# Kernel optimization log

Hardware: AMD Instinct MI355X
Metric: run time of the kernel (lower is better)

The kernel has to match this reference:

```python
import jax, jax.numpy as jnp
import numpy as np

N_NODES = 16384
N_EDGES = 262144
D_IN = 256
D = 256          # out_feats == d_model
H = 512          # d_inner = 2*d_model
E = 64           # moe_num_expert
TOP_K = 2
CAP = 1024       # expert capacity = 2 * N*K / E (generous, no drops in practice)
BN_EPS = 1e-5


def setup_inputs() -> dict:
    key = jax.random.key(0)
    ks = jax.random.split(key, 16)
    s = lambda d: 1.0 / np.sqrt(d)
    inp = {
        "feats": jax.random.normal(ks[0], (N_NODES, D_IN), jnp.float32),
        "W_gc": jax.random.normal(ks[1], (D_IN, D), jnp.float32) * s(D_IN),
        "b_gc": jnp.zeros((D,), jnp.float32),
        "W_res": jax.random.normal(ks[2], (D_IN, D), jnp.float32) * s(D_IN),
        "b_res": jnp.zeros((D,), jnp.float32),
        "Wg": jax.random.normal(ks[3], (D, E), jnp.float32) * s(D),
        "bg": jnp.zeros((E,), jnp.float32),
        "w1": jax.random.normal(ks[4], (E, D, H), jnp.float32) * s(D),
        "b1": jnp.zeros((E, H), jnp.float32),
        "w2": jax.random.normal(ks[5], (E, H, D), jnp.float32) * s(H),
        "b2": jnp.zeros((E, D), jnp.float32),
        "gamma": jnp.ones((D,), jnp.float32),
        "beta": jnp.zeros((D,), jnp.float32),
        "src": jax.random.randint(ks[6], (N_EDGES,), 0, N_NODES),
        "dst": jax.random.randint(ks[7], (N_EDGES,), 0, N_NODES),
    }
    return inp


def _moe_ff(x, Wg, bg, w1, b1, w2, b2):
    """Top-2 MoE FFN (FMoE NaiveGate semantics): softmax over selected top-k logits."""
    N = x.shape[0]
    logits = x @ Wg + bg                                   # [N, E]
    vals, idx = jax.lax.top_k(logits, TOP_K)               # [N, K]
    gates = jax.nn.softmax(vals, axis=-1)                  # [N, K]

    e_flat = idx.reshape(-1)                               # [N*K]
    g_flat = gates.reshape(-1)
    tok = jnp.arange(N * TOP_K) // TOP_K                   # token id per pair

    order = jnp.argsort(e_flat)                            # stable sort by expert
    e_s, tok_s, g_s = e_flat[order], tok[order], g_flat[order]
    counts = jnp.bincount(e_flat, length=E)
    offs = jnp.concatenate([jnp.zeros((1,), counts.dtype), jnp.cumsum(counts)[:-1]])
    rank = jnp.arange(N * TOP_K) - offs[e_s]               # position within expert
    valid = rank < CAP
    slot = jnp.where(valid, e_s * CAP + rank, E * CAP)     # overflow -> dummy row

    buf = jnp.zeros((E * CAP + 1, D), x.dtype).at[slot].set(x[tok_s])
    h = buf[: E * CAP].reshape(E, CAP, D)
    h1 = jax.nn.gelu(jnp.einsum("ecd,edh->ech", h, w1) + b1[:, None, :], approximate=False)
    h2 = jnp.einsum("ech,ehd->ecd", h1, w2) + b2[:, None, :]
    out_buf = h2.reshape(E * CAP, D)

    y_s = jnp.where(valid[:, None], out_buf[jnp.minimum(slot, E * CAP - 1)], 0.0)
    return jnp.zeros((N, D), x.dtype).at[tok_s].add(g_s[:, None] * y_s)


def _forward(feats, W_gc, b_gc, W_res, b_res, Wg, bg, w1, b1, w2, b2, gamma, beta, src, dst):
    n = feats.shape[0]
    ones = jnp.ones((src.shape[0],), feats.dtype)
    deg_out = jnp.clip(jax.ops.segment_sum(ones, src, num_segments=n), 1.0)
    deg_in = jnp.clip(jax.ops.segment_sum(ones, dst, num_segments=n), 1.0)
    # symmetric-normalized GCN aggregation over edge list
    h = feats * jax.lax.rsqrt(deg_out)[:, None]
    m = jax.ops.segment_sum(h[src], dst, num_segments=n) * jax.lax.rsqrt(deg_in)[:, None]
    gc = m @ W_gc + b_gc
    x = gc + (feats @ W_res + b_res)                       # residual branch (dropout p=0)

    core = _moe_ff(x, Wg, bg, w1, b1, w2, b2)
    y = x + core                                           # pre-BN residual
    mean = jnp.mean(y, axis=0)
    var = jnp.mean((y - mean) ** 2, axis=0)                # biased var (torch BN train)
    return (y - mean) * jax.lax.rsqrt(var + BN_EPS) * gamma + beta


def reference(feats, W_gc, b_gc, W_res, b_res, Wg, bg, w1, b1, w2, b2, gamma, beta, src, dst):
    return _forward(feats, W_gc, b_gc, W_res, b_res, Wg, bg, w1, b1, w2, b2, gamma, beta, src, dst)
```

## Files before the change

### kernel.cpp

```cpp
#include <hip/hip_runtime.h>
#include <math.h>

static const int kN     = 16384;
static const int kEdges = 262144;
static const int kD     = 256;
static const int kH     = 512;
static const int kE     = 64;
static const int kCap   = 1024;
static const int kPairs = kN * 2;

static const size_t OFF_DEGO    = 0;
static const size_t OFF_DEGI    = OFF_DEGO + 65536;
static const size_t OFF_CURSOR  = OFF_DEGI + 65536;
static const size_t OFF_ECOUNT  = OFF_CURSOR + 65536;
static const size_t OFF_ECUR    = OFF_ECOUNT + 256;
static const size_t OFF_COLSUM  = OFF_ECUR + 256;
static const size_t OFF_COLSUM2 = OFF_COLSUM + 1024;
static const size_t ZERO_BYTES  = OFF_COLSUM2 + 1024;
static const size_t OFF_EOFFS   = ZERO_BYTES;
static const size_t OFF_CSROFF  = OFF_EOFFS + 512;
static const size_t OFF_CSRSRC  = OFF_CSROFF + 65792;
static const size_t OFF_PLIST   = OFF_CSRSRC + 1048576;
static const size_t OFF_EIDX    = OFF_PLIST + 131072;
static const size_t OFF_EGATE   = OFF_EIDX + 131072;
static const size_t OFF_SCALE   = OFF_EGATE + 131072;
static const size_t OFF_SHIFT   = OFF_SCALE + 1024;
static const size_t OFF_OSC     = OFF_SHIFT + 1024;
static const size_t OFF_ISC     = OFF_OSC + 65536;
static const size_t OFF_WQ1     = OFF_ISC + 65536;
static const size_t OFF_WQ2     = OFF_WQ1 + 65536;
static const size_t OFF_BGE     = OFF_WQ2 + 65536;
static const size_t OFF_WCAT    = OFF_BGE + 256;
static const size_t OFF_M       = OFF_WCAT + 262144;
static const size_t OFF_X       = OFF_M + 16777216;
static const size_t OFF_XB      = OFF_X + 16777216;
static const size_t OFF_LOGITS  = OFF_XB + 8388608;
static const size_t OFF_POUT    = OFF_LOGITS + 4194304;
static const size_t OFF_W1T     = OFF_POUT + 16777216;
static const size_t OFF_W2T     = OFF_W1T + 16777216;
static const size_t OFF_H1B     = OFF_W2T + 16777216;
static const size_t OFF_PART1   = OFF_H1B + 33554432;
static const size_t OFF_PART2   = OFF_PART1 + 262144;

typedef __bf16 bfrag __attribute__((ext_vector_type(8)));
typedef float f32x4 __attribute__((ext_vector_type(4)));

__device__ __forceinline__ float gelu_f(float v) {
    float u = v * (0.7978845608f + 0.0356774081f * v * v);
    float t = __expf(-2.0f * fabsf(u));
    float th = (1.0f - t) * __builtin_amdgcn_rcpf(1.0f + t);
    th = copysignf(th, u);
    return 0.5f * v * (1.0f + th);
}
__device__ __forceinline__ unsigned short f2bf(float f) {
    union { float f; unsigned int u; } v; v.f = f;
    unsigned int u = v.u;
    unsigned int r = (u + 0x7FFFu + ((u >> 16) & 1u)) >> 16;
    return (unsigned short)r;
}
__device__ __forceinline__ float bf2f(unsigned short s) {
    union { unsigned int u; float f; } v; v.u = ((unsigned int)s) << 16;
    return v.f;
}

__global__ __launch_bounds__(256) void k_count_deg(const int* __restrict__ src,
                                                   const int* __restrict__ dst,
                                                   int* __restrict__ dego,
                                                   int* __restrict__ degi) {
    int i = blockIdx.x * 256 + threadIdx.x;
    if (i < kEdges) {
        atomicAdd(&dego[src[i]], 1);
        atomicAdd(&degi[dst[i]], 1);
    }
}

__global__ __launch_bounds__(256) void k_scales(const int* __restrict__ dego,
                                                const int* __restrict__ degi,
                                                float* __restrict__ osc,
                                                float* __restrict__ isc) {
    int i = blockIdx.x * 256 + threadIdx.x;
    int a = dego[i]; if (a < 1) a = 1;
    int b = degi[i]; if (b < 1) b = 1;
    osc[i] = rsqrtf((float)a);
    isc[i] = rsqrtf((float)b);
}

__global__ __launch_bounds__(1024) void k_scan_nodes(const int* __restrict__ degi,
                                                     int* __restrict__ offs) {
    __shared__ int sums[1024];
    int t = threadIdx.x;
    int base = t * 16;
    int loc[16];
    int s = 0;
#pragma unroll
    for (int i = 0; i < 16; ++i) { loc[i] = degi[base + i]; s += loc[i]; }
    sums[t] = s;
    __syncthreads();
    for (int off = 1; off < 1024; off <<= 1) {
        int v = (t >= off) ? sums[t - off] : 0;
        __syncthreads();
        sums[t] += v;
        __syncthreads();
    }
    int run = sums[t] - s;
#pragma unroll
    for (int i = 0; i < 16; ++i) { offs[base + i] = run; run += loc[i]; }
    if (t == 1023) offs[kN] = run;
}

__global__ __launch_bounds__(256) void k_build_csr(const int* __restrict__ src,
                                                   const int* __restrict__ dst,
                                                   const int* __restrict__ offs,
                                                   int* __restrict__ cursor,
                                                   int* __restrict__ csr_src) {
    int i = blockIdx.x * 256 + threadIdx.x;
    if (i < kEdges) {
        int d = dst[i];
        int pos = atomicAdd(&cursor[d], 1);
        csr_src[offs[d] + pos] = src[i];
    }
}

__global__ __launch_bounds__(256) void k_aggregate(const float* __restrict__ feats,
                                                   const float* __restrict__ osc,
                                                   const float* __restrict__ isc,
                                                   const int* __restrict__ offs,
                                                   const int* __restrict__ csr_src,
                                                   float* __restrict__ m) {
    __shared__ f32x4 red[256];
    int n = blockIdx.x;
    int t = threadIdx.x;
    int c4 = (t & 63) * 4;
    int es = t >> 6;
    int beg = offs[n], end = offs[n + 1];
    f32x4 acc = {0.f, 0.f, 0.f, 0.f};
    for (int i = beg + es; i < end; i += 4) {
        int s = csr_src[i];
        float sc = osc[s];
        const float4 v = *(const float4*)(feats + (size_t)s * kD + c4);
        acc[0] += v.x * sc; acc[1] += v.y * sc;
        acc[2] += v.z * sc; acc[3] += v.w * sc;
    }
    red[t] = acc;
    __syncthreads();
    if (t < 64) {
        f32x4 a = red[t], b = red[t + 64], c = red[t + 128], d = red[t + 192];
        float si = isc[n];
        float4 o;
        o.x = (a[0] + b[0] + c[0] + d[0]) * si;
        o.y = (a[1] + b[1] + c[1] + d[1]) * si;
        o.z = (a[2] + b[2] + c[2] + d[2]) * si;
        o.w = (a[3] + b[3] + c[3] + d[3]) * si;
        *(float4*)(m + (size_t)n * kD + c4) = o;
    }
}

__global__ __launch_bounds__(256) void k_compose(const float* __restrict__ Wgc,
                                                 const float* __restrict__ Wres,
                                                 const float* __restrict__ Wg,
                                                 const float* __restrict__ bgc,
                                                 const float* __restrict__ bres,
                                                 const float* __restrict__ bg,
                                                 float* __restrict__ Wq1,
                                                 float* __restrict__ Wq2,
                                                 float* __restrict__ bge) {
    int tid = blockIdx.x * 256 + threadIdx.x;
    if (tid < 2 * kD * kE) {
        int mat = tid >> 14;
        int rem = tid & 16383;
        int d = rem >> 6, e = rem & 63;
        const float* A = mat ? Wres : Wgc;
        float acc = 0.f;
        for (int c = 0; c < kD; ++c)
            acc = fmaf(A[d * kD + c], Wg[c * kE + e], acc);
        (mat ? Wq2 : Wq1)[d * kE + e] = acc;
    } else if (tid < 2 * kD * kE + kE) {
        int e = tid - 2 * kD * kE;
        float acc = bg[e];
        for (int d = 0; d < kD; ++d)
            acc = fmaf(bgc[d] + bres[d], Wg[d * kE + e], acc);
        bge[e] = acc;
    }
}

#define FMA16()                                                                         \
    acc[0][0]=fmaf(a.x,b.x,acc[0][0]); acc[0][1]=fmaf(a.x,b.y,acc[0][1]);               \
    acc[0][2]=fmaf(a.x,b.z,acc[0][2]); acc[0][3]=fmaf(a.x,b.w,acc[0][3]);               \
    acc[1][0]=fmaf(a.y,b.x,acc[1][0]); acc[1][1]=fmaf(a.y,b.y,acc[1][1]);               \
    acc[1][2]=fmaf(a.y,b.z,acc[1][2]); acc[1][3]=fmaf(a.y,b.w,acc[1][3]);               \
    acc[2][0]=fmaf(a.z,b.x,acc[2][0]); acc[2][1]=fmaf(a.z,b.y,acc[2][1]);               \
    acc[2][2]=fmaf(a.z,b.z,acc[2][2]); acc[2][3]=fmaf(a.z,b.w,acc[2][3]);               \
    acc[3][0]=fmaf(a.w,b.x,acc[3][0]); acc[3][1]=fmaf(a.w,b.y,acc[3][1]);               \
    acc[3][2]=fmaf(a.w,b.z,acc[3][2]); acc[3][3]=fmaf(a.w,b.w,acc[3][3]);

__global__ __launch_bounds__(256) void k_gate_comp(const float* __restrict__ m,
                                                   const float* __restrict__ feats,
                                                   const float* __restrict__ Wq1,
                                                   const float* __restrict__ Wq2,
                                                   const float* __restrict__ bge,
                                                   float* __restrict__ logits) {
    __shared__ float As[32][68];
    __shared__ float Bs[32][68];
    const int t = threadIdx.x;
    const int tx = t & 15, ty = t >> 4;
    const int m0 = blockIdx.y * 64;
    float acc[4][4] = {};
    for (int pass = 0; pass < 2; ++pass) {
        const float* A = pass ? feats : m;
        const float* B = pass ? Wq2 : Wq1;
        for (int kb = 0; kb < kD; kb += 32) {
            __syncthreads();
#pragma unroll
            for (int i = 0; i < 2; ++i) {
                int fidx = i * 256 + t;
                int r = fidx >> 3, k4 = fidx & 7;
                float4 v = *(const float4*)(A + (size_t)(m0 + r) * kD + kb + k4 * 4);
                As[k4 * 4 + 0][r] = v.x; As[k4 * 4 + 1][r] = v.y;
                As[k4 * 4 + 2][r] = v.z; As[k4 * 4 + 3][r] = v.w;
            }
#pragma unroll
            for (int i = 0; i < 2; ++i) {
                int fidx = i * 256 + t;
                int kk = fidx >> 4, c4 = fidx & 15;
                float4 v = *(const float4*)(B + (size_t)(kb + kk) * kE + c4 * 4);
                *(float4*)&Bs[kk][c4 * 4] = v;
            }
            __syncthreads();
#pragma unroll
            for (int kk = 0; kk < 32; ++kk) {
                float4 a = *(const float4*)&As[kk][ty * 4];
                float4 b = *(const float4*)&Bs[kk][tx * 4];
                FMA16();
            }
        }
    }
    int col0 = tx * 4;
    float4 bb = *(const float4*)(bge + col0);
#pragma unroll
    for (int i = 0; i < 4; ++i) {
        int row = m0 + ty * 4 + i;
        float4 o;
        o.x = acc[i][0] + bb.x; o.y = acc[i][1] + bb.y;
        o.z = acc[i][2] + bb.z; o.w = acc[i][3] + bb.w;
        *(float4*)(logits + (size_t)row * kE + col0) = o;
    }
}

__global__ __launch_bounds__(256) void k_cast_cat(const float* __restrict__ m,
                                                  const float* __restrict__ feats,
                                                  unsigned short* __restrict__ acat) {
    int i = blockIdx.x * 256 + threadIdx.x;
    const float* srcp = blockIdx.y ? feats : m;
    int doff = blockIdx.y ? 256 : 0;
    size_t g = (size_t)i * 8;
    int tok = (int)(g >> 8), d = (int)(g & 255);
    float4 a = *(const float4*)(srcp + g);
    float4 b = *(const float4*)(srcp + g + 4);
    ushort4 o0, o1;
    o0.x = f2bf(a.x); o0.y = f2bf(a.y); o0.z = f2bf(a.z); o0.w = f2bf(a.w);
    o1.x = f2bf(b.x); o1.y = f2bf(b.y); o1.z = f2bf(b.z); o1.w = f2bf(b.w);
    unsigned short* dstp = acat + (size_t)tok * 512 + doff + d;
    *(ushort4*)dstp = o0;
    *(ushort4*)(dstp + 4) = o1;
}

__global__ __launch_bounds__(256) void k_transpose_cast(const float* __restrict__ w,
                                                        unsigned short* __restrict__ wt,
                                                        int R, int C, int dstride, int doff) {
    __shared__ unsigned short tile[64][65];
    int e = blockIdx.z;
    const float* W = w + (size_t)e * R * C;
    unsigned short* WT = wt + (size_t)e * R * C;
    int r0 = blockIdx.y * 64, c0 = blockIdx.x * 64;
    int t = threadIdx.x;
#pragma unroll
    for (int i = 0; i < 4; ++i) {
        int idx = i * 256 + t;
        int r = idx >> 4, c4 = idx & 15;
        float4 v = *(const float4*)(W + (size_t)(r0 + r) * C + c0 + c4 * 4);
        tile[r][c4 * 4 + 0] = f2bf(v.x); tile[r][c4 * 4 + 1] = f2bf(v.y);
        tile[r][c4 * 4 + 2] = f2bf(v.z); tile[r][c4 * 4 + 3] = f2bf(v.w);
    }
    __syncthreads();
#pragma unroll
    for (int i = 0; i < 4; ++i) {
        int idx = i * 256 + t;
        int c = idx >> 4, r4 = idx & 15;
        ushort4 o;
        o.x = tile[r4 * 4 + 0][c]; o.y = tile[r4 * 4 + 1][c];
        o.z = tile[r4 * 4 + 2][c]; o.w = tile[r4 * 4 + 3][c];
        *(ushort4*)(WT + (size_t)(c0 + c) * dstride + doff + r0 + r4 * 4) = o;
    }
}

__global__ __launch_bounds__(256) void k_xgemm_mfma(const unsigned short* __restrict__ acat,
                                                    const unsigned short* __restrict__ wcat,
                                                    const float* __restrict__ bgc,
                                                    const float* __restrict__ bres,
                                                    float* __restrict__ x,
                                                    unsigned short* __restrict__ xb) {
    __shared__ unsigned short As[128 * 32];
    __shared__ unsigned short Bs[128 * 32];
    const int t = threadIdx.x;
    const int m0 = blockIdx.y * 128;
    const int n0 = blockIdx.x * 128;
    const int lane = t & 63, w = t >> 6;
    const int m_off = (w & 1) * 64, n_off = (w >> 1) * 64;
    const int quad = lane >> 4, lr = lane & 15;
    float breg[4];
#pragma unroll
    for (int ni = 0; ni < 4; ++ni) {
        int col = n0 + n_off + ni * 16 + lr;
        breg[ni] = bgc[col] + bres[col];
    }
    const int arow0 = t >> 2, arow1 = 64 + (t >> 2);
    const int kseg = (t & 3) * 8;
    const unsigned short* pA0 = acat + (size_t)(m0 + arow0) * 512 + kseg;
    const unsigned short* pA1 = acat + (size_t)(m0 + arow1) * 512 + kseg;
    const unsigned short* pB0 = wcat + (size_t)(n0 + arow0) * 512 + kseg;
    const unsigned short* pB1 = wcat + (size_t)(n0 + arow1) * 512 + kseg;
    unsigned short* sA0 = &As[arow0 * 32 + kseg];
    unsigned short* sA1 = &As[arow1 * 32 + kseg];
    unsigned short* sB0 = &Bs[arow0 * 32 + kseg];
    unsigned short* sB1 = &Bs[arow1 * 32 + kseg];
    f32x4 acc[4][4] = {};
    for (int kb = 0; kb < 512; kb += 32) {
        uint4 a0 = *(const uint4*)(pA0 + kb);
        uint4 a1 = *(const uint4*)(pA1 + kb);
        uint4 bv0 = *(const uint4*)(pB0 + kb);
        uint4 bv1 = *(const uint4*)(pB1 + kb);
        __syncthreads();
        *(uint4*)sA0 = a0; *(uint4*)sA1 = a1;
        *(uint4*)sB0 = bv0; *(uint4*)sB1 = bv1;
        __syncthreads();
        bfrag af[4], bf[4];
#pragma unroll
        for (int mi = 0; mi < 4; ++mi)
            af[mi] = *(const bfrag*)&As[(m_off + mi * 16 + lr) * 32 + quad * 8];
#pragma unroll
        for (int ni = 0; ni < 4; ++ni)
            bf[ni] = *(const bfrag*)&Bs[(n_off + ni * 16 + lr) * 32 + quad * 8];
#pragma unroll
        for (int mi = 0; mi < 4; ++mi)
#pragma unroll
            for (int ni = 0; ni < 4; ++ni)
                acc[mi][ni] = __builtin_amdgcn_mfma_f32_16x16x32_bf16(af[mi], bf[ni], acc[mi][ni], 0, 0, 0);
    }
#pragma unroll
    for (int mi = 0; mi < 4; ++mi) {
#pragma unroll
        for (int r = 0; r < 4; ++r) {
            int row = m0 + m_off + mi * 16 + quad * 4 + r;
            float* xrow = x + (size_t)row * kD + n0 + n_off + lr;
            unsigned short* xbrow = xb + (size_t)row * kD + n0 + n_off + lr;
#pragma unroll
            for (int ni = 0; ni < 4; ++ni) {
                float v = acc[mi][ni][r] + breg[ni];
                xrow[ni * 16] = v;
                xbrow[ni * 16] = f2bf(v);
            }
        }
    }
}

__global__ __launch_bounds__(256) void k_topk(const float* __restrict__ logits,
                                              int* __restrict__ eidx,
                                              float* __restrict__ egate,
                                              int* __restrict__ ecount) {
    __shared__ int hist[kE];
    int t = threadIdx.x;
    int n = blockIdx.x * 256 + t;
    if (t < kE) hist[t] = 0;
    __syncthreads();
    const float* row = logits + (size_t)n * kE;
    float v0 = -3.4e38f, v1 = -3.4e38f;
    int i0 = 0, i1 = 0;
    for (int e4 = 0; e4 < kE; e4 += 4) {
        float4 vv = *(const float4*)(row + e4);
        float vs[4] = {vv.x, vv.y, vv.z, vv.w};
#pragma unroll
        for (int j = 0; j < 4; ++j) {
            float v = vs[j];
            int e = e4 + j;
            if (v > v0) { v1 = v0; i1 = i0; v0 = v; i0 = e; }
            else if (v > v1) { v1 = v; i1 = e; }
        }
    }
    float ex = expf(v1 - v0);
    float g0 = 1.0f / (1.0f + ex);
    float g1 = ex * g0;
    eidx[2 * n] = i0; eidx[2 * n + 1] = i1;
    egate[2 * n] = g0; egate[2 * n + 1] = g1;
    atomicAdd(&hist[i0], 1);
    atomicAdd(&hist[i1], 1);
    __syncthreads();
    if (t < kE) {
        int c = hist[t];
        if (c > 0) atomicAdd(&ecount[t], c);
    }
}

__global__ void k_scan_experts(const int* __restrict__ ecount, int* __restrict__ eoffs) {
    if (threadIdx.x == 0) {
        int s = 0;
        for (int e = 0; e < kE; ++e) { eoffs[e] = s; s += ecount[e]; }
        eoffs[kE] = s;
    }
}

__global__ __launch_bounds__(256) void k_scatter(const int* __restrict__ eidx,
                                                 const int* __restrict__ eoffs,
                                                 int* __restrict__ ecur,
                                                 int* __restrict__ plist) {
    __shared__ int lh[kE];
    __shared__ int gbase[kE];
    int t = threadIdx.x;
    int p0 = blockIdx.x * 512 + t;
    if (t < kE) lh[t] = 0;
    __syncthreads();
    int e0 = eidx[p0], e1 = eidx[p0 + 256];
    atomicAdd(&lh[e0], 1);
    atomicAdd(&lh[e1], 1);
    __syncthreads();
    if (t < kE) {
        int c = lh[t];
        int b = (c > 0) ? atomicAdd(&ecur[t], c) : 0;
        gbase[t] = eoffs[t] + b;
        lh[t] = 0;
    }
    __syncthreads();
    int r0 = atomicAdd(&lh[e0], 1);
    int r1 = atomicAdd(&lh[e1], 1);
    plist[gbase[e0] + r0] = p0;
    plist[gbase[e1] + r1] = p0 + 256;
}

__global__ __launch_bounds__(256) void k_moe1_mfma(const unsigned short* __restrict__ xb,
                                                   const unsigned short* __restrict__ w1t,
                                                   const float* __restrict__ b1,
                                                   const int* __restrict__ plist,
                                                   const int* __restrict__ eoffs,
                                                   const int* __restrict__ ecount,
                                                   unsigned short* __restrict__ h1b) {
    __shared__ unsigned short As[128 * 32];
    __shared__ unsigned short Bs[128 * 32];
    __shared__ int rowtok[128];
    const int e = blockIdx.z;
    int cnt = ecount[e]; if (cnt > kCap) cnt = kCap;
    const int m0 = blockIdx.y * 128;
    if (m0 >= cnt) return;
    const int n0 = blockIdx.x * 128;
    const int base = eoffs[e];
    const int t = threadIdx.x;
    if (t < 128) {
        int slot = m0 + t;
        rowtok[t] = (slot < cnt) ? (plist[base + slot] >> 1) : -1;
    }
    const int lane = t & 63, w = t >> 6;
    const int m_off = (w & 1) * 64, n_off = (w >> 1) * 64;
    const int quad = lane >> 4, lr = lane & 15;
    const unsigned short* Bbase = w1t + (size_t)e * kH * kD;
    float breg[4];
#pragma unroll
    for (int ni = 0; ni < 4; ++ni) breg[ni] = b1[e * kH + n0 + n_off + ni * 16 + lr];
    const int arow0 = t >> 2, arow1 = 64 + (t >> 2);
    const int kseg = (t & 3) * 8;
    __syncthreads();
    const int tok0 = rowtok[arow0], tok1 = rowtok[arow1];
    const unsigned short* pA0 = (tok0 >= 0) ? xb + (size_t)tok0 * kD + kseg : nullptr;
    const unsigned short* pA1 = (tok1 >= 0) ? xb + (size_t)tok1 * kD + kseg : nullptr;
    const unsigned short* pB0 = Bbase + (size_t)(n0 + arow0) * kD + kseg;
    const unsigned short* pB1 = Bbase + (size_t)(n0 + arow1) * kD + kseg;
    unsigned short* sA0 = &As[arow0 * 32 + kseg];
    unsigned short* sA1 = &As[arow1 * 32 + kseg];
    unsigned short* sB0 = &Bs[arow0 * 32 + kseg];
    unsigned short* sB1 = &Bs[arow1 * 32 + kseg];
    f32x4 acc[4][4] = {};
    for (int kb = 0; kb < kD; kb += 32) {
        uint4 a0 = pA0 ? *(const uint4*)(pA0 + kb) : make_uint4(0, 0, 0, 0);
        uint4 a1 = pA1 ? *(const uint4*)(pA1 + kb) : make_uint4(0, 0, 0, 0);
        uint4 bv0 = *(const uint4*)(pB0 + kb);
        uint4 bv1 = *(const uint4*)(pB1 + kb);
        __syncthreads();
        *(uint4*)sA0 = a0; *(uint4*)sA1 = a1;
        *(uint4*)sB0 = bv0; *(uint4*)sB1 = bv1;
        __syncthreads();
        bfrag af[4], bf[4];
#pragma unroll
        for (int mi = 0; mi < 4; ++mi)
            af[mi] = *(const bfrag*)&As[(m_off + mi * 16 + lr) * 32 + quad * 8];
#pragma unroll
        for (int ni = 0; ni < 4; ++ni)
            bf[ni] = *(const bfrag*)&Bs[(n_off + ni * 16 + lr) * 32 + quad * 8];
#pragma unroll
        for (int mi = 0; mi < 4; ++mi)
#pragma unroll
            for (int ni = 0; ni < 4; ++ni)
                acc[mi][ni] = __builtin_amdgcn_mfma_f32_16x16x32_bf16(af[mi], bf[ni], acc[mi][ni], 0, 0, 0);
    }
#pragma unroll
    for (int mi = 0; mi < 4; ++mi) {
#pragma unroll
        for (int r = 0; r < 4; ++r) {
            int slot = m0 + m_off + mi * 16 + quad * 4 + r;
            if (slot < cnt) {
                unsigned short* orow = h1b + (size_t)(base + slot) * kH + n0 + n_off + lr;
#pragma unroll
                for (int ni = 0; ni < 4; ++ni)
                    orow[ni * 16] = f2bf(gelu_f(acc[mi][ni][r] + breg[ni]));
            }
        }
    }
}

__global__ __launch_bounds__(256) void k_moe2_mfma(const unsigned short* __restrict__ h1b,
                                                   const unsigned short* __restrict__ w2t,
                                                   const float* __restrict__ b2,
                                                   const int* __restrict__ plist,
                                                   const int* __restrict__ eoffs,
                                                   const int* __restrict__ ecount,
                                                   const float* __restrict__ egate,
                                                   unsigned short* __restrict__ pout) {
    __shared__ unsigned short As[128 * 32];
    __shared__ unsigned short Bs[128 * 32];
    __shared__ int prow[128];
    __shared__ float sgate[128];
    const int e = blockIdx.z;
    int cnt = ecount[e]; if (cnt > kCap) cnt = kCap;
    const int m0 = blockIdx.y * 128;
    if (m0 >= cnt) return;
    const int n0 = blockIdx.x * 128;
    const int base = eoffs[e];
    const int t = threadIdx.x;
    if (t < 128) {
        int slot = m0 + t;
        int p = (slot < cnt) ? plist[base + slot] : -1;
        prow[t] = p;
        sgate[t] = (p >= 0) ? egate[p] : 0.f;
    }
    const int lane = t & 63, w = t >> 6;
    const int m_off = (w & 1) * 64, n_off = (w >> 1) * 64;
    const int quad = lane >> 4, lr = lane & 15;
    const unsigned short* Bbase = w2t + (size_t)e * kD * kH;
    float breg[4];
#pragma unroll
    for (int ni = 0; ni < 4; ++ni) breg[ni] = b2[e * kD + n0 + n_off + ni * 16 + lr];
    const int arow0 = t >> 2, arow1 = 64 + (t >> 2);
    const int kseg = (t & 3) * 8;
    int aslot0 = m0 + arow0, aslot1 = m0 + arow1;
    const unsigned short* pA0 = (aslot0 < cnt) ? h1b + (size_t)(base + aslot0) * kH + kseg : nullptr;
    const unsigned short* pA1 = (aslot1 < cnt) ? h1b + (size_t)(base + aslot1) * kH + kseg : nullptr;
    const unsigned short* pB0 = Bbase + (size_t)(n0 + arow0) * kH + kseg;
    const unsigned short* pB1 = Bbase + (size_t)(n0 + arow1) * kH + kseg;
    unsigned short* sA0 = &As[arow0 * 32 + kseg];
    unsigned short* sA1 = &As[arow1 * 32 + kseg];
    unsigned short* sB0 = &Bs[arow0 * 32 + kseg];
    unsigned short* sB1 = &Bs[arow1 * 32 + kseg];
    f32x4 acc[4][4] = {};
    for (int kb = 0; kb < kH; kb += 32) {
        uint4 a0 = pA0 ? *(const uint4*)(pA0 + kb) : make_uint4(0, 0, 0, 0);
        uint4 a1 = pA1 ? *(const uint4*)(pA1 + kb) : make_uint4(0, 0, 0, 0);
        uint4 bv0 = *(const uint4*)(pB0 + kb);
        uint4 bv1 = *(const uint4*)(pB1 + kb);
        __syncthreads();
        *(uint4*)sA0 = a0; *(uint4*)sA1 = a1;
        *(uint4*)sB0 = bv0; *(uint4*)sB1 = bv1;
        __syncthreads();
        bfrag af[4], bf[4];
#pragma unroll
        for (int mi = 0; mi < 4; ++mi)
            af[mi] = *(const bfrag*)&As[(m_off + mi * 16 + lr) * 32 + quad * 8];
#pragma unroll
        for (int ni = 0; ni < 4; ++ni)
            bf[ni] = *(const bfrag*)&Bs[(n_off + ni * 16 + lr) * 32 + quad * 8];
#pragma unroll
        for (int mi = 0; mi < 4; ++mi)
#pragma unroll
            for (int ni = 0; ni < 4; ++ni)
                acc[mi][ni] = __builtin_amdgcn_mfma_f32_16x16x32_bf16(af[mi], bf[ni], acc[mi][ni], 0, 0, 0);
    }
#pragma unroll
    for (int mi = 0; mi < 4; ++mi) {
#pragma unroll
        for (int r = 0; r < 4; ++r) {
            int lslot = m_off + mi * 16 + quad * 4 + r;
            int p = prow[lslot];
            if (p >= 0) {
                float g = sgate[lslot];
                unsigned short* orow = pout + (size_t)p * kD + n0 + n_off + lr;
#pragma unroll
                for (int ni = 0; ni < 4; ++ni)
                    orow[ni * 16] = f2bf(g * (acc[mi][ni][r] + breg[ni]));
            }
        }
    }
}

__global__ __launch_bounds__(256) void k_colsum(const float* __restrict__ x,
                                                const unsigned short* __restrict__ pout,
                                                float* __restrict__ part1,
                                                float* __restrict__ part2) {
    int d = threadIdx.x;
    int r0 = blockIdx.x * 64;
    float s = 0.f, s2 = 0.f;
    for (int i = 0; i < 64; ++i) {
        int row = r0 + i;
        float v = x[(size_t)row * kD + d]
                + bf2f(pout[(size_t)(2 * row) * kD + d])
                + bf2f(pout[(size_t)(2 * row + 1) * kD + d]);
        s += v; s2 += v * v;
    }
    part1[blockIdx.x * kD + d] = s;
    part2[blockIdx.x * kD + d] = s2;
}

__global__ void k_bnparams(const float* __restrict__ part1,
                           const float* __restrict__ part2,
                           const float* __restrict__ gamma,
                           const float* __restrict__ beta,
                           float* __restrict__ scale,
                           float* __restrict__ shift) {
    int d = threadIdx.x;
    float s = 0.f, s2 = 0.f;
    for (int b = 0; b < 256; ++b) {
        s += part1[b * kD + d];
        s2 += part2[b * kD + d];
    }
    float mean = s * (1.0f / kN);
    float var = s2 * (1.0f / kN) - mean * mean;
    float inv = rsqrtf(var + 1e-5f);
    float sc = inv * gamma[d];
    scale[d] = sc;
    shift[d] = beta[d] - mean * sc;
}

__global__ __launch_bounds__(256) void k_apply2(const float* __restrict__ x,
                                                const unsigned short* __restrict__ pout,
                                                const float* __restrict__ scale,
                                                const float* __restrict__ shift,
                                                float* __restrict__ out) {
    int i = blockIdx.x * 256 + threadIdx.x;
    size_t g = (size_t)i * 4;
    int row = (int)(g >> 8);
    int d = (int)(g & 255);
    float4 v = *(const float4*)(x + g);
    ushort4 p0 = *(const ushort4*)(pout + (size_t)(2 * row) * kD + d);
    ushort4 p1 = *(const ushort4*)(pout + (size_t)(2 * row + 1) * kD + d);
    v.x += bf2f(p0.x) + bf2f(p1.x);
    v.y += bf2f(p0.y) + bf2f(p1.y);
    v.z += bf2f(p0.z) + bf2f(p1.z);
    v.w += bf2f(p0.w) + bf2f(p1.w);
    float4 sc = *(const float4*)(scale + d);
    float4 sh = *(const float4*)(shift + d);
    v.x = v.x * sc.x + sh.x;
    v.y = v.y * sc.y + sh.y;
    v.z = v.z * sc.z + sh.z;
    v.w = v.w * sc.w + sh.w;
    *(float4*)(out + g) = v;
}

extern "C" void kernel_launch(void* const* d_in, const int* in_sizes, int n_in,
                              void* d_out, int out_size, void* d_ws, size_t ws_size,
                              hipStream_t stream) {
    const float* feats = (const float*)d_in[0];
    const float* Wgc   = (const float*)d_in[1];
    const float* bgc   = (const float*)d_in[2];
    const float* Wres  = (const float*)d_in[3];
    const float* bres  = (const float*)d_in[4];
    const float* Wg    = (const float*)d_in[5];
    const float* bg    = (const float*)d_in[6];
    const float* w1    = (const float*)d_in[7];
    const float* b1    = (const float*)d_in[8];
    const float* w2    = (const float*)d_in[9];
    const float* b2    = (const float*)d_in[10];
    const float* gamma = (const float*)d_in[11];
    const float* beta  = (const float*)d_in[12];
    const int*   src   = (const int*)d_in[13];
    const int*   dst   = (const int*)d_in[14];

    char* ws = (char*)d_ws;
    int*   dego    = (int*)(ws + OFF_DEGO);
    int*   degi    = (int*)(ws + OFF_DEGI);
    int*   cursor  = (int*)(ws + OFF_CURSOR);
    int*   ecount  = (int*)(ws + OFF_ECOUNT);
    int*   ecur    = (int*)(ws + OFF_ECUR);
    int*   eoffs   = (int*)(ws + OFF_EOFFS);
    int*   csroff  = (int*)(ws + OFF_CSROFF);
    int*   csrsrc  = (int*)(ws + OFF_CSRSRC);
    int*   plist   = (int*)(ws + OFF_PLIST);
    int*   eidx    = (int*)(ws + OFF_EIDX);
    float* egate   = (float*)(ws + OFF_EGATE);
    float* scale   = (float*)(ws + OFF_SCALE);
    float* shift   = (float*)(ws + OFF_SHIFT);
    float* osc     = (float*)(ws + OFF_OSC);
    float* iscv    = (float*)(ws + OFF_ISC);
    float* Wq1     = (float*)(ws + OFF_WQ1);
    float* Wq2     = (float*)(ws + OFF_WQ2);
    float* bge     = (float*)(ws + OFF_BGE);
    unsigned short* wcat = (unsigned short*)(ws + OFF_WCAT);
    float* mbuf    = (float*)(ws + OFF_M);
    float* xbuf    = (float*)(ws + OFF_X);
    unsigned short* xb   = (unsigned short*)(ws + OFF_XB);
    float* logits  = (float*)(ws + OFF_LOGITS);
    unsigned short* pout = (unsigned short*)(ws + OFF_POUT);
    unsigned short* acat = (unsigned short*)(ws + OFF_POUT);
    unsigned short* w1t  = (unsigned short*)(ws + OFF_W1T);
    unsigned short* w2t  = (unsigned short*)(ws + OFF_W2T);
    unsigned short* h1b  = (unsigned short*)(ws + OFF_H1B);
    float* part1   = (float*)(ws + OFF_PART1);
    float* part2   = (float*)(ws + OFF_PART2);

    hipMemsetAsync(ws, 0, ZERO_BYTES, stream);

    k_transpose_cast<<<dim3(kH / 64, kD / 64, kE), 256, 0, stream>>>(w1, w1t, kD, kH, kD, 0);
    k_transpose_cast<<<dim3(kD / 64, kH / 64, kE), 256, 0, stream>>>(w2, w2t, kH, kD, kH, 0);
    k_transpose_cast<<<dim3(kD / 64, kD / 64, 1), 256, 0, stream>>>(Wgc, wcat, kD, kD, 512, 0);
    k_transpose_cast<<<dim3(kD / 64, kD / 64, 1), 256, 0, stream>>>(Wres, wcat, kD, kD, 512, 256);
    k_compose<<<129, 256, 0, stream>>>(Wgc, Wres, Wg, bgc, bres, bg, Wq1, Wq2, bge);
    k_count_deg<<<kEdges / 256, 256, 0, stream>>>(src, dst, dego, degi);
    k_scales<<<kN / 256, 256, 0, stream>>>(dego, degi, osc, iscv);
    k_scan_nodes<<<1, 1024, 0, stream>>>(degi, csroff);
    k_build_csr<<<kEdges / 256, 256, 0, stream>>>(src, dst, csroff, cursor, csrsrc);
    k_aggregate<<<kN, 256, 0, stream>>>(feats, osc, iscv, csroff, csrsrc, mbuf);
    k_gate_comp<<<dim3(1, kN / 64), 256, 0, stream>>>(mbuf, feats, Wq1, Wq2, bge, logits);
    k_cast_cat<<<dim3(kN * kD / 8 / 256, 2), 256, 0, stream>>>(mbuf, feats, acat);
    k_xgemm_mfma<<<dim3(kD / 128, kN / 128), 256, 0, stream>>>(acat, wcat, bgc, bres, xbuf, xb);
    k_topk<<<kN / 256, 256, 0, stream>>>(logits, eidx, egate, ecount);
    k_scan_experts<<<1, 64, 0, stream>>>(ecount, eoffs);
    k_scatter<<<kPairs / 512, 256, 0, stream>>>(eidx, eoffs, ecur, plist);
    k_moe1_mfma<<<dim3(kH / 128, kCap / 128, kE), 256, 0, stream>>>(xb, w1t, b1, plist, eoffs, ecount, h1b);
    k_moe2_mfma<<<dim3(kD / 128, kCap / 128, kE), 256, 0, stream>>>(h1b, w2t, b2, plist, eoffs, ecount, egate, pout);
    k_colsum<<<kN / 64, 256, 0, stream>>>(xbuf, pout, part1, part2);
    k_bnparams<<<1, 256, 0, stream>>>(part1, part2, gamma, beta, scale, shift);
    k_apply2<<<(kN * kD / 4) / 256, 256, 0, stream>>>(xbuf, pout, scale, shift, (float*)d_out);
}
```

Baseline: 414.2 us.

## Use direct global-to-LDS loads with swizzled 64-wide K tiles in GEMMs, fuse cast into aggregate

The three MFMA GEMMs now stage A and B tiles with global_load_lds straight into LDS, using a K tile of 64 and an XOR swizzle to avoid bank conflicts. Padding rows read from a zeroed workspace row, so the null-pointer branches are gone. The aggregation kernel now uses 512 threads and writes the bf16 copy of m directly, with a separate small kernel casting feats, which removes the combined cast pass over m. The trade-offs are twice the LDS per block, which may lower occupancy, and a loop that is still not double-buffered.

```diff
diff --git a/kernel.cpp b/kernel.cpp
--- a/kernel.cpp
+++ b/kernel.cpp
@@ -14,9 +14,8 @@
 static const size_t OFF_CURSOR  = OFF_DEGI + 65536;
 static const size_t OFF_ECOUNT  = OFF_CURSOR + 65536;
 static const size_t OFF_ECUR    = OFF_ECOUNT + 256;
-static const size_t OFF_COLSUM  = OFF_ECUR + 256;
-static const size_t OFF_COLSUM2 = OFF_COLSUM + 1024;
-static const size_t ZERO_BYTES  = OFF_COLSUM2 + 1024;
+static const size_t OFF_ZROW    = OFF_ECUR + 256;
+static const size_t ZERO_BYTES  = OFF_ZROW + 2048;
 static const size_t OFF_EOFFS   = ZERO_BYTES;
 static const size_t OFF_CSROFF  = OFF_EOFFS + 512;
 static const size_t OFF_CSRSRC  = OFF_CSROFF + 65792;
@@ -45,6 +44,12 @@
 typedef __bf16 bfrag __attribute__((ext_vector_type(8)));
 typedef float f32x4 __attribute__((ext_vector_type(4)));
 
+__device__ __forceinline__ void gll16(const void* g, void* l) {
+    __builtin_amdgcn_global_load_lds(
+        (const __attribute__((address_space(1))) unsigned int*)g,
+        (__attribute__((address_space(3))) unsigned int*)l, 16, 0, 0);
+}
+
 __device__ __forceinline__ float gelu_f(float v) {
     float u = v * (0.7978845608f + 0.0356774081f * v * v);
     float t = __expf(-2.0f * fabsf(u));
@@ -121,20 +126,21 @@
     }
 }
 
-__global__ __launch_bounds__(256) void k_aggregate(const float* __restrict__ feats,
+__global__ __launch_bounds__(512) void k_aggregate(const float* __restrict__ feats,
                                                    const float* __restrict__ osc,
                                                    const float* __restrict__ isc,
                                                    const int* __restrict__ offs,
                                                    const int* __restrict__ csr_src,
-                                                   float* __restrict__ m) {
-    __shared__ f32x4 red[256];
+                                                   float* __restrict__ m,
+                                                   unsigned short* __restrict__ acat) {
+    __shared__ f32x4 red[512];
     int n = blockIdx.x;
     int t = threadIdx.x;
     int c4 = (t & 63) * 4;
     int es = t >> 6;
     int beg = offs[n], end = offs[n + 1];
     f32x4 acc = {0.f, 0.f, 0.f, 0.f};
-    for (int i = beg + es; i < end; i += 4) {
+    for (int i = beg + es; i < end; i += 8) {
         int s = csr_src[i];
         float sc = osc[s];
         const float4 v = *(const float4*)(feats + (size_t)s * kD + c4);
@@ -144,15 +150,35 @@
     red[t] = acc;
     __syncthreads();
     if (t < 64) {
-        f32x4 a = red[t], b = red[t + 64], c = red[t + 128], d = red[t + 192];
+        f32x4 a = red[t];
+#pragma unroll
+        for (int j = 1; j < 8; ++j) {
+            f32x4 b = red[t + 64 * j];
+            a[0] += b[0]; a[1] += b[1]; a[2] += b[2]; a[3] += b[3];
+        }
         float si = isc[n];
         float4 o;
-        o.x = (a[0] + b[0] + c[0] + d[0]) * si;
-        o.y = (a[1] + b[1] + c[1] + d[1]) * si;
-        o.z = (a[2] + b[2] + c[2] + d[2]) * si;
-        o.w = (a[3] + b[3] + c[3] + d[3]) * si;
+        o.x = a[0] * si; o.y = a[1] * si; o.z = a[2] * si; o.w = a[3] * si;
         *(float4*)(m + (size_t)n * kD + c4) = o;
-    }
+        ushort4 ob;
+        ob.x = f2bf(o.x); ob.y = f2bf(o.y); ob.z = f2bf(o.z); ob.w = f2bf(o.w);
+        *(ushort4*)(acat + (size_t)n * 512 + c4) = ob;
+    }
+}
+
+__global__ __launch_bounds__(256) void k_cast_feats(const float* __restrict__ feats,
+                                                    unsigned short* __restrict__ acat) {
+    int i = blockIdx.x * 256 + threadIdx.x;
+    size_t g = (size_t)i * 8;
+    int tok = (int)(g >> 8), d = (int)(g & 255);
+    float4 a = *(const float4*)(feats + g);
+    float4 b = *(const float4*)(feats + g + 4);
+    ushort4 o0, o1;
+    o0.x = f2bf(a.x); o0.y = f2bf(a.y); o0.z = f2bf(a.z); o0.w = f2bf(a.w);
+    o1.x = f2bf(b.x); o1.y = f2bf(b.y); o1.z = f2bf(b.z); o1.w = f2bf(b.w);
+    unsigned short* dstp = acat + (size_t)tok * 512 + 256 + d;
+    *(ushort4*)dstp = o0;
+    *(ushort4*)(dstp + 4) = o1;
 }
 
 __global__ __launch_bounds__(256) void k_compose(const float* __restrict__ Wgc,
@@ -246,24 +272,6 @@
     }
 }
 
-__global__ __launch_bounds__(256) void k_cast_cat(const float* __restrict__ m,
-                                                  const float* __restrict__ feats,
-                                                  unsigned short* __restrict__ acat) {
-    int i = blockIdx.x * 256 + threadIdx.x;
-    const float* srcp = blockIdx.y ? feats : m;
-    int doff = blockIdx.y ? 256 : 0;
-    size_t g = (size_t)i * 8;
-    int tok = (int)(g >> 8), d = (int)(g & 255);
-    float4 a = *(const float4*)(srcp + g);
-    float4 b = *(const float4*)(srcp + g + 4);
-    ushort4 o0, o1;
-    o0.x = f2bf(a.x); o0.y = f2bf(a.y); o0.z = f2bf(a.z); o0.w = f2bf(a.w);
-    o1.x = f2bf(b.x); o1.y = f2bf(b.y); o1.z = f2bf(b.z); o1.w = f2bf(b.w);
-    unsigned short* dstp = acat + (size_t)tok * 512 + doff + d;
-    *(ushort4*)dstp = o0;
-    *(ushort4*)(dstp + 4) = o1;
-}
-
 __global__ __launch_bounds__(256) void k_transpose_cast(const float* __restrict__ w,
                                                         unsigned short* __restrict__ wt,
                                                         int R, int C, int dstride, int doff) {
@@ -299,11 +307,10 @@
                                                     const float* __restrict__ bres,
                                                     float* __restrict__ x,
                                                     unsigned short* __restrict__ xb) {
-    __shared__ unsigned short As[128 * 32];
-    __shared__ unsigned short Bs[128 * 32];
+    __shared__ unsigned short As[128 * 64];
+    __shared__ unsigned short Bs[128 * 64];
     const int t = threadIdx.x;
-    const int m0 = blockIdx.y * 128;
-    const int n0 = blockIdx.x * 128;
+    const int m0 = blockIdx.y * 128, n0 = blockIdx.x * 128;
     const int lane = t & 63, w = t >> 6;
     const int m_off = (w & 1) * 64, n_off = (w >> 1) * 64;
     const int quad = lane >> 4, lr = lane & 15;
@@ -313,38 +320,37 @@
         int col = n0 + n_off + ni * 16 + lr;
         breg[ni] = bgc[col] + bres[col];
     }
-    const int arow0 = t >> 2, arow1 = 64 + (t >> 2);
-    const int kseg = (t & 3) * 8;
-    const unsigned short* pA0 = acat + (size_t)(m0 + arow0) * 512 + kseg;
-    const unsigned short* pA1 = acat + (size_t)(m0 + arow1) * 512 + kseg;
-    const unsigned short* pB0 = wcat + (size_t)(n0 + arow0) * 512 + kseg;
-    const unsigned short* pB1 = wcat + (size_t)(n0 + arow1) * 512 + kseg;
-    unsigned short* sA0 = &As[arow0 * 32 + kseg];
-    unsigned short* sA1 = &As[arow1 * 32 + kseg];
-    unsigned short* sB0 = &Bs[arow0 * 32 + kseg];
-    unsigned short* sB1 = &Bs[arow1 * 32 + kseg];
+    const int lsub = lane >> 3, lslot = lane & 7;
+    const int swz8 = (lslot ^ lsub) * 8;
+    const unsigned short* pAb = acat + (size_t)(m0 + w * 8 + lsub) * 512 + swz8;
+    const unsigned short* pBb = wcat + (size_t)(n0 + w * 8 + lsub) * 512 + swz8;
+    unsigned short* sA = As + w * 8 * 64;
+    unsigned short* sB = Bs + w * 8 * 64;
     f32x4 acc[4][4] = {};
-    for (int kb = 0; kb < 512; kb += 32) {
-        uint4 a0 = *(const uint4*)(pA0 + kb);
-        uint4 a1 = *(const uint4*)(pA1 + kb);
-        uint4 bv0 = *(const uint4*)(pB0 + kb);
-        uint4 bv1 = *(const uint4*)(pB1 + kb);
+    for (int kb = 0; kb < 512; kb += 64) {
         __syncthreads();
-        *(uint4*)sA0 = a0; *(uint4*)sA1 = a1;
-        *(uint4*)sB0 = bv0; *(uint4*)sB1 = bv1;
+#pragma unroll
+        for (int j = 0; j < 4; ++j) {
+            gll16(pAb + (size_t)j * 32 * 512 + kb, sA + j * 2048);
+            gll16(pBb + (size_t)j * 32 * 512 + kb, sB + j * 2048);
+        }
         __syncthreads();
-        bfrag af[4], bf[4];
-#pragma unroll
-        for (int mi = 0; mi < 4; ++mi)
-            af[mi] = *(const bfrag*)&As[(m_off + mi * 16 + lr) * 32 + quad * 8];
-#pragma unroll
-        for (int ni = 0; ni < 4; ++ni)
-            bf[ni] = *(const bfrag*)&Bs[(n_off + ni * 16 + lr) * 32 + quad * 8];
-#pragma unroll
-        for (int mi = 0; mi < 4; ++mi)
+#pragma unroll
+        for (int h = 0; h < 2; ++h) {
+            const int soff = ((h * 4 + quad) ^ (lr & 7)) * 8;
+            bfrag af[4], bf[4];
+#pragma unroll
+            for (int mi = 0; mi < 4; ++mi)
+                af[mi] = *(const bfrag*)&As[(m_off + mi * 16 + lr) * 64 + soff];
 #pragma unroll
             for (int ni = 0; ni < 4; ++ni)
-                acc[mi][ni] = __builtin_amdgcn_mfma_f32_16x16x32_bf16(af[mi], bf[ni], acc[mi][ni], 0, 0, 0);
+                bf[ni] = *(const bfrag*)&Bs[(n_off + ni * 16 + lr) * 64 + soff];
+#pragma unroll
+            for (int mi = 0; mi < 4; ++mi)
+#pragma unroll
+                for (int ni = 0; ni < 4; ++ni)
+                    acc[mi][ni] = __builtin_amdgcn_mfma_f32_16x16x32_bf16(af[mi], bf[ni], acc[mi][ni], 0, 0, 0);
+        }
     }
 #pragma unroll
     for (int mi = 0; mi < 4; ++mi) {
@@ -441,9 +447,10 @@
                                                    const int* __restrict__ plist,
                                                    const int* __restrict__ eoffs,
                                                    const int* __restrict__ ecount,
+                                                   const unsigned short* __restrict__ zrow,
                                                    unsigned short* __restrict__ h1b) {
-    __shared__ unsigned short As[128 * 32];
-    __shared__ unsigned short Bs[128 * 32];
+    __shared__ unsigned short As[128 * 64];
+    __shared__ unsigned short Bs[128 * 64];
     __shared__ int rowtok[128];
     const int e = blockIdx.z;
     int cnt = ecount[e]; if (cnt > kCap) cnt = kCap;
@@ -463,40 +470,44 @@
     float breg[4];
 #pragma unroll
     for (int ni = 0; ni < 4; ++ni) breg[ni] = b1[e * kH + n0 + n_off + ni * 16 + lr];
-    const int arow0 = t >> 2, arow1 = 64 + (t >> 2);
-    const int kseg = (t & 3) * 8;
-    __syncthreads();
-    const int tok0 = rowtok[arow0], tok1 = rowtok[arow1];
-    const unsigned short* pA0 = (tok0 >= 0) ? xb + (size_t)tok0 * kD + kseg : nullptr;
-    const unsigned short* pA1 = (tok1 >= 0) ? xb + (size_t)tok1 * kD + kseg : nullptr;
-    const unsigned short* pB0 = Bbase + (size_t)(n0 + arow0) * kD + kseg;
-    const unsigned short* pB1 = Bbase + (size_t)(n0 + arow1) * kD + kseg;
-    unsigned short* sA0 = &As[arow0 * 32 + kseg];
-    unsigned short* sA1 = &As[arow1 * 32 + kseg];
-    unsigned short* sB0 = &Bs[arow0 * 32 + kseg];
-    unsigned short* sB1 = &Bs[arow1 * 32 + kseg];
+    const int lsub = lane >> 3, lslot = lane & 7;
+    const int swz8 = (lslot ^ lsub) * 8;
+    __syncthreads();
+    const unsigned short* pA[4];
+#pragma unroll
+    for (int j = 0; j < 4; ++j) {
+        int r = w * 8 + j * 32 + lsub;
+        int tok = rowtok[r];
+        pA[j] = (tok >= 0) ? (xb + (size_t)tok * kD + swz8) : (zrow + swz8);
+    }
+    const unsigned short* pBb = Bbase + (size_t)(n0 + w * 8 + lsub) * kD + swz8;
+    unsigned short* sA = As + w * 8 * 64;
+    unsigned short* sB = Bs + w * 8 * 64;
     f32x4 acc[4][4] = {};
-    for (int kb = 0; kb < kD; kb += 32) {
-        uint4 a0 = pA0 ? *(const uint4*)(pA0 + kb) : make_uint4(0, 0, 0, 0);
-        uint4 a1 = pA1 ? *(const uint4*)(pA1 + kb) : make_uint4(0, 0, 0, 0);
-        uint4 bv0 = *(const uint4*)(pB0 + kb);
-        uint4 bv1 = *(const uint4*)(pB1 + kb);
+    for (int kb = 0; kb < kD; kb += 64) {
         __syncthreads();
-        *(uint4*)sA0 = a0; *(uint4*)sA1 = a1;
-        *(uint4*)sB0 = bv0; *(uint4*)sB1 = bv1;
+#pragma unroll
+        for (int j = 0; j < 4; ++j) {
+            gll16(pA[j] + kb, sA + j * 2048);
+            gll16(pBb + (size_t)j * 32 * kD + kb, sB + j * 2048);
+        }
         __syncthreads();
-        bfrag af[4], bf[4];
-#pragma unroll
-        for (int mi = 0; mi < 4; ++mi)
-            af[mi] = *(const bfrag*)&As[(m_off + mi * 16 + lr) * 32 + quad * 8];
-#pragma unroll
-        for (int ni = 0; ni < 4; ++ni)
-            bf[ni] = *(const bfrag*)&Bs[(n_off + ni * 16 + lr) * 32 + quad * 8];
-#pragma unroll
-        for (int mi = 0; mi < 4; ++mi)
+#pragma unroll
+        for (int h = 0; h < 2; ++h) {
+            const int soff = ((h * 4 + quad) ^ (lr & 7)) * 8;
+            bfrag af[4], bf[4];
+#pragma unroll
+            for (int mi = 0; mi < 4; ++mi)
+                af[mi] = *(const bfrag*)&As[(m_off + mi * 16 + lr) * 64 + soff];
 #pragma unroll
             for (int ni = 0; ni < 4; ++ni)
-                acc[mi][ni] = __builtin_amdgcn_mfma_f32_16x16x32_bf16(af[mi], bf[ni], acc[mi][ni], 0, 0, 0);
+                bf[ni] = *(const bfrag*)&Bs[(n_off + ni * 16 + lr) * 64 + soff];
+#pragma unroll
+            for (int mi = 0; mi < 4; ++mi)
+#pragma unroll
+                for (int ni = 0; ni < 4; ++ni)
+                    acc[mi][ni] = __builtin_amdgcn_mfma_f32_16x16x32_bf16(af[mi], bf[ni], acc[mi][ni], 0, 0, 0);
+        }
     }
 #pragma unroll
     for (int mi = 0; mi < 4; ++mi) {
@@ -520,9 +531,10 @@
                                                    const int* __restrict__ eoffs,
                                                    const int* __restrict__ ecount,
                                                    const float* __restrict__ egate,
+                                                   const unsigned short* __restrict__ zrow,
                                                    unsigned short* __restrict__ pout) {
-    __shared__ unsigned short As[128 * 32];
-    __shared__ unsigned short Bs[128 * 32];
+    __shared__ unsigned short As[128 * 64];
+    __shared__ unsigned short Bs[128 * 64];
     __shared__ int prow[128];
     __shared__ float sgate[128];
     const int e = blockIdx.z;
@@ -545,48 +557,52 @@
     float breg[4];
 #pragma unroll
     for (int ni = 0; ni < 4; ++ni) breg[ni] = b2[e * kD + n0 + n_off + ni * 16 + lr];
-    const int arow0 = t >> 2, arow1 = 64 + (t >> 2);
-    const int kseg = (t & 3) * 8;
-    int aslot0 = m0 + arow0, aslot1 = m0 + arow1;
-    const unsigned short* pA0 = (aslot0 < cnt) ? h1b + (size_t)(base + aslot0) * kH + kseg : nullptr;
-    const unsigned short* pA1 = (aslot1 < cnt) ? h1b + (size_t)(base + aslot1) * kH + kseg : nullptr;
-    const unsigned short* pB0 = Bbase + (size_t)(n0 + arow0) * kH + kseg;
-    const unsigned short* pB1 = Bbase + (size_t)(n0 + arow1) * kH + kseg;
-    unsigned short* sA0 = &As[arow0 * 32 + kseg];
-    unsigned short* sA1 = &As[arow1 * 32 + kseg];
-    unsigned short* sB0 = &Bs[arow0 * 32 + kseg];
-    unsigned short* sB1 = &Bs[arow1 * 32 + kseg];
+    const int lsub = lane >> 3, lslot = lane & 7;
+    const int swz8 = (lslot ^ lsub) * 8;
+    const unsigned short* pA[4];
+#pragma unroll
+    for (int j = 0; j < 4; ++j) {
+        int r = w * 8 + j * 32 + lsub;
+        int slot = m0 + r;
+        pA[j] = (slot < cnt) ? (h1b + (size_t)(base + slot) * kH + swz8) : (zrow + swz8);
+    }
+    const unsigned short* pBb = Bbase + (size_t)(n0 + w * 8 + lsub) * kH + swz8;
+    unsigned short* sA = As + w * 8 * 64;
+    unsigned short* sB = Bs + w * 8 * 64;
     f32x4 acc[4][4] = {};
-    for (int kb = 0; kb < kH; kb += 32) {
-        uint4 a0 = pA0 ? *(const uint4*)(pA0 + kb) : make_uint4(0, 0, 0, 0);
-        uint4 a1 = pA1 ? *(const uint4*)(pA1 + kb) : make_uint4(0, 0, 0, 0);
-        uint4 bv0 = *(const uint4*)(pB0 + kb);
-        uint4 bv1 = *(const uint4*)(pB1 + kb);
+    for (int kb = 0; kb < kH; kb += 64) {
         __syncthreads();
-        *(uint4*)sA0 = a0; *(uint4*)sA1 = a1;
-        *(uint4*)sB0 = bv0; *(uint4*)sB1 = bv1;
+#pragma unroll
+        for (int j = 0; j < 4; ++j) {
+            gll16(pA[j] + kb, sA + j * 2048);
+            gll16(pBb + (size_t)j * 32 * kH + kb, sB + j * 2048);
+        }
         __syncthreads();
-        bfrag af[4], bf[4];
-#pragma unroll
-        for (int mi = 0; mi < 4; ++mi)
-            af[mi] = *(const bfrag*)&As[(m_off + mi * 16 + lr) * 32 + quad * 8];
-#pragma unroll
-        for (int ni = 0; ni < 4; ++ni)
-            bf[ni] = *(const bfrag*)&Bs[(n_off + ni * 16 + lr) * 32 + quad * 8];
-#pragma unroll
-        for (int mi = 0; mi < 4; ++mi)
+#pragma unroll
+        for (int h = 0; h < 2; ++h) {
+            const int soff = ((h * 4 + quad) ^ (lr & 7)) * 8;
+            bfrag af[4], bf[4];
+#pragma unroll
+            for (int mi = 0; mi < 4; ++mi)
+                af[mi] = *(const bfrag*)&As[(m_off + mi * 16 + lr) * 64 + soff];
 #pragma unroll
             for (int ni = 0; ni < 4; ++ni)
-                acc[mi][ni] = __builtin_amdgcn_mfma_f32_16x16x32_bf16(af[mi], bf[ni], acc[mi][ni], 0, 0, 0);
+                bf[ni] = *(const bfrag*)&Bs[(n_off + ni * 16 + lr) * 64 + soff];
+#pragma unroll
+            for (int mi = 0; mi < 4; ++mi)
+#pragma unroll
+                for (int ni = 0; ni < 4; ++ni)
+                    acc[mi][ni] = __builtin_amdgcn_mfma_f32_16x16x32_bf16(af[mi], bf[ni], acc[mi][ni], 0, 0, 0);
+        }
     }
 #pragma unroll
     for (int mi = 0; mi < 4; ++mi) {
 #pragma unroll
         for (int r = 0; r < 4; ++r) {
-            int lslot = m_off + mi * 16 + quad * 4 + r;
-            int p = prow[lslot];
+            int lslot2 = m_off + mi * 16 + quad * 4 + r;
+            int p = prow[lslot2];
             if (p >= 0) {
-                float g = sgate[lslot];
+                float g = sgate[lslot2];
                 unsigned short* orow = pout + (size_t)p * kD + n0 + n_off + lr;
 #pragma unroll
                 for (int ni = 0; ni < 4; ++ni)
@@ -684,6 +700,7 @@
     int*   cursor  = (int*)(ws + OFF_CURSOR);
     int*   ecount  = (int*)(ws + OFF_ECOUNT);
     int*   ecur    = (int*)(ws + OFF_ECUR);
+    const unsigned short* zrow = (const unsigned short*)(ws + OFF_ZROW);
     int*   eoffs   = (int*)(ws + OFF_EOFFS);
     int*   csroff  = (int*)(ws + OFF_CSROFF);
     int*   csrsrc  = (int*)(ws + OFF_CSRSRC);
@@ -721,15 +738,15 @@
     k_scales<<<kN / 256, 256, 0, stream>>>(dego, degi, osc, iscv);
     k_scan_nodes<<<1, 1024, 0, stream>>>(degi, csroff);
     k_build_csr<<<kEdges / 256, 256, 0, stream>>>(src, dst, csroff, cursor, csrsrc);
-    k_aggregate<<<kN, 256, 0, stream>>>(feats, osc, iscv, csroff, csrsrc, mbuf);
+    k_cast_feats<<<kN * kD / 8 / 256, 256, 0, stream>>>(feats, acat);
+    k_aggregate<<<kN, 512, 0, stream>>>(feats, osc, iscv, csroff, csrsrc, mbuf, acat);
     k_gate_comp<<<dim3(1, kN / 64), 256, 0, stream>>>(mbuf, feats, Wq1, Wq2, bge, logits);
-    k_cast_cat<<<dim3(kN * kD / 8 / 256, 2), 256, 0, stream>>>(mbuf, feats, acat);
     k_xgemm_mfma<<<dim3(kD / 128, kN / 128), 256, 0, stream>>>(acat, wcat, bgc, bres, xbuf, xb);
     k_topk<<<kN / 256, 256, 0, stream>>>(logits, eidx, egate, ecount);
     k_scan_experts<<<1, 64, 0, stream>>>(ecount, eoffs);
     k_scatter<<<kPairs / 512, 256, 0, stream>>>(eidx, eoffs, ecur, plist);
-    k_moe1_mfma<<<dim3(kH / 128, kCap / 128, kE), 256, 0, stream>>>(xb, w1t, b1, plist, eoffs, ecount, h1b);
-    k_moe2_mfma<<<dim3(kD / 128, kCap / 128, kE), 256, 0, stream>>>(h1b, w2t, b2, plist, eoffs, ecount, egate, pout);
+    k_moe1_mfma<<<dim3(kH / 128, kCap / 128, kE), 256, 0, stream>>>(xb, w1t, b1, plist, eoffs, ecount, zrow, h1b);
+    k_moe2_mfma<<<dim3(kD / 128, kCap / 128, kE), 256, 0, stream>>>(h1b, w2t, b2, plist, eoffs, ecount, egate, zrow, pout);
     k_colsum<<<kN / 64, 256, 0, stream>>>(xbuf, pout, part1, part2);
     k_bnparams<<<1, 256, 0, stream>>>(part1, part2, gamma, beta, scale, shift);
     k_apply2<<<(kN * kD / 4) / 256, 256, 0, stream>>>(xbuf, pout, scale, shift, (float*)d_out);
```

Result: no change. 408.4 us (-1.4%).
